# Optimization experiments

Measured on AMD Instinct MI355X. Metric: run time of the kernel, lower is better.

The kernel has to match this reference:

```python
import jax, jax.numpy as jnp
import numpy as np

EPS = 1e-5

def ter_quant(w):
    # BitNet b1.58 absmean ternary quantization: scale by mean(|W|), round to {-1,0,1}, rescale.
    gamma = jnp.mean(jnp.abs(w)) + EPS
    wq = jnp.clip(jnp.round(w / gamma), -1.0, 1.0) * gamma
    return wq

def setup_inputs() -> dict:
    key = jax.random.key(0)
    k_x, k_w1, k_w2 = jax.random.split(key, 3)
    B, S, D, H = 64, 197, 768, 3072
    x = jax.random.normal(k_x, (B, S, D), dtype=jnp.float32)
    w1 = jax.random.normal(k_w1, (H, D), dtype=jnp.float32) * (1.0 / np.sqrt(D))
    b1 = jnp.zeros((H,), dtype=jnp.float32)
    w2 = jax.random.normal(k_w2, (D, H), dtype=jnp.float32) * (1.0 / np.sqrt(H))
    b2 = jnp.zeros((D,), dtype=jnp.float32)
    return {"x": x, "w1": w1, "b1": b1, "w2": w2, "b2": b2}

def reference(x, w1, b1, w2, b2):
    # fc1: ternary-quantized linear, exact GELU, fc2: ternary-quantized linear (dropout p=0 is identity)
    h = jnp.einsum('bsd,hd->bsh', x, ter_quant(w1)) + b1
    h = jax.nn.gelu(h, approximate=False)
    y = jnp.einsum('bsh,dh->bsd', h, ter_quant(w2)) + b2
    return y
```

## Files before the change

kernel.cpp:

```cpp
#include <hip/hip_runtime.h>
#include <hip/hip_bf16.h>
#include <math.h>

typedef __bf16 bf16_t;
typedef __bf16 bf16x8 __attribute__((ext_vector_type(8)));
typedef float f32x4 __attribute__((ext_vector_type(4)));

#define QEPS 1e-5

__device__ __forceinline__ void gload_lds16(const void* g, void* l) {
  __builtin_amdgcn_global_load_lds((const __attribute__((address_space(1))) void*)g,
                                   (__attribute__((address_space(3))) void*)l, 16, 0, 0);
}

__device__ __forceinline__ float gelu_exact(float x) {
  float a = x * 0.7071067811865476f;
  float s = fabsf(a);
  float t = __builtin_amdgcn_rcpf(__builtin_fmaf(0.3275911f, s, 1.0f));
  float p = __builtin_fmaf(1.061405429f, t, -1.453152027f);
  p = __builtin_fmaf(p, t, 1.421413741f);
  p = __builtin_fmaf(p, t, -0.284496736f);
  p = __builtin_fmaf(p, t, 0.254829592f);
  p = p * t;
  float e = __expf(-s * s);
  float er = copysignf(__builtin_fmaf(-p, e, 1.0f), a);
  return 0.5f * x * (1.0f + er);
}

__global__ void reduce_part_kernel(const float* __restrict__ w1, const float* __restrict__ w2,
                                   int n, double* __restrict__ part) {
  const bool second = blockIdx.x >= 256;
  const float* __restrict__ w = second ? w2 : w1;
  const int b = second ? blockIdx.x - 256 : blockIdx.x;
  double s = 0.0;
  const int stride = 256 * 256 * 4;
  for (int i = (b * 256 + threadIdx.x) * 4; i < n; i += stride) {
    float4 v = *(const float4*)(w + i);
    s += (double)fabsf(v.x) + (double)fabsf(v.y) + (double)fabsf(v.z) + (double)fabsf(v.w);
  }
  for (int off = 32; off > 0; off >>= 1)
    s += __shfl_down(s, off, 64);
  __shared__ double ls[4];
  int lane = threadIdx.x & 63, wv = threadIdx.x >> 6;
  if (lane == 0) ls[wv] = s;
  __syncthreads();
  if (threadIdx.x == 0) part[blockIdx.x] = ls[0] + ls[1] + ls[2] + ls[3];
}

__global__ void prep_kernel(const float* __restrict__ w1, const float* __restrict__ w2,
                            const float* __restrict__ x, const double* __restrict__ part,
                            double* __restrict__ gammas, bf16_t* __restrict__ q1,
                            bf16_t* __restrict__ q2, bf16_t* __restrict__ xb) {
  const int tid = threadIdx.x;
  const int b = blockIdx.x;
  if (b < 2304) {
    const bool second = b >= 1152;
    double p = part[(second ? 256 : 0) + tid];
    for (int off = 32; off > 0; off >>= 1)
      p += __shfl_down(p, off, 64);
    __shared__ double red[4];
    if ((tid & 63) == 0) red[tid >> 6] = p;
    __syncthreads();
    const double g = (red[0] + red[1] + red[2] + red[3]) / 2359296.0 + QEPS;
    if (tid == 0 && (b == 0 || b == 1152)) gammas[second ? 1 : 0] = g;
    const double rg = 1.0 / g;
    const int gchunk = (second ? b - 1152 : b) * 256 + tid;
    const int tile = gchunk >> 10, cidx = gchunk & 1023;
    const int r = cidx >> 3, slot = cidx & 7, kc = slot ^ (r & 7);
    int row, col, C;
    const float* __restrict__ W;
    if (second) { C = 3072; W = w2; row = (tile / 48) * 128 + r; col = (tile % 48) * 64 + kc * 8; }
    else        { C = 768;  W = w1; row = (tile / 12) * 128 + r; col = (tile % 12) * 64 + kc * 8; }
    const float4 v0 = *(const float4*)(W + (size_t)row * C + col);
    const float4 v1 = *(const float4*)(W + (size_t)row * C + col + 4);
    bf16x8 o;
    o[0] = (bf16_t)(float)fmin(1.0, fmax(-1.0, rint((double)v0.x * rg)));
    o[1] = (bf16_t)(float)fmin(1.0, fmax(-1.0, rint((double)v0.y * rg)));
    o[2] = (bf16_t)(float)fmin(1.0, fmax(-1.0, rint((double)v0.z * rg)));
    o[3] = (bf16_t)(float)fmin(1.0, fmax(-1.0, rint((double)v0.w * rg)));
    o[4] = (bf16_t)(float)fmin(1.0, fmax(-1.0, rint((double)v1.x * rg)));
    o[5] = (bf16_t)(float)fmin(1.0, fmax(-1.0, rint((double)v1.y * rg)));
    o[6] = (bf16_t)(float)fmin(1.0, fmax(-1.0, rint((double)v1.z * rg)));
    o[7] = (bf16_t)(float)fmin(1.0, fmax(-1.0, rint((double)v1.w * rg)));
    *(bf16x8*)((second ? q2 : q1) + (size_t)gchunk * 8) = o;
  } else {
    const int gchunk = (b - 2304) * 256 + tid;
    const int tile = gchunk >> 10, cidx = gchunk & 1023;
    const int r = cidx >> 3, slot = cidx & 7, kc = slot ^ (r & 7);
    const int row = (tile / 12) * 128 + r;
    const int col = (tile % 12) * 64 + kc * 8;
    bf16x8 o;
    if (row < 12608) {
      const float4 v0 = *(const float4*)(x + (size_t)row * 768 + col);
      const float4 v1 = *(const float4*)(x + (size_t)row * 768 + col + 4);
      o[0] = (bf16_t)v0.x; o[1] = (bf16_t)v0.y; o[2] = (bf16_t)v0.z; o[3] = (bf16_t)v0.w;
      o[4] = (bf16_t)v1.x; o[5] = (bf16_t)v1.y; o[6] = (bf16_t)v1.z; o[7] = (bf16_t)v1.w;
    } else {
      o = bf16x8{};
    }
    *(bf16x8*)(xb + (size_t)gchunk * 8) = o;
  }
}

template <int EPI>
__global__ __launch_bounds__(256, 2)
void gemm_db(const bf16_t* __restrict__ A, const bf16_t* __restrict__ B,
             const float* __restrict__ bias, const double* __restrict__ gptr,
             void* __restrict__ Cout, int nkt, int gx, int Mvalid, int aux) {
  extern __shared__ bf16_t sm[];

  const int G = gridDim.x;
  const int f = blockIdx.x;
  const int xcd = f & 7;
  const int idx = f >> 3;
  const int q8 = G >> 3, r8 = G & 7;
  const int t = xcd * q8 + (xcd < r8 ? xcd : r8) + idx;
  const int bx = t % gx;
  const int by = t / gx;

  const int tid = threadIdx.x;
  const int lane = tid & 63;
  const int wave = tid >> 6;
  const int row16 = lane & 15;
  const int quad = lane >> 4;
  const int wr = (wave >> 1) * 64;
  const int wc = (wave & 1) * 64;
  const int sw0 = (quad ^ (row16 & 7)) * 8;
  const int sw1 = sw0 ^ 32;

  const bf16_t* const gA = A + (size_t)by * nkt * 8192;
  const bf16_t* const gB = B + (size_t)bx * nkt * 8192;

  f32x4 acc[4][4] = {};

  const int o8 = tid * 8;
  const int w512 = wave * 512;

#pragma unroll
  for (int l = 0; l < 4; l++) {
    gload_lds16(gA + l * 2048 + o8, sm + l * 2048 + w512);
    gload_lds16(gB + l * 2048 + o8, sm + 16384 + l * 2048 + w512);
  }
  __syncthreads();

  int p = 0;
  for (int T = 0; T < nkt; T++) {
    if (T + 1 < nkt) {
      const bf16_t* sa = gA + (size_t)(T + 1) * 8192;
      const bf16_t* sb = gB + (size_t)(T + 1) * 8192;
      bf16_t* dA = sm + (p ^ 1) * 8192;
      bf16_t* dB = sm + 16384 + (p ^ 1) * 8192;
#pragma unroll
      for (int l = 0; l < 4; l++) {
        gload_lds16(sa + l * 2048 + o8, dA + l * 2048 + w512);
        gload_lds16(sb + l * 2048 + o8, dB + l * 2048 + w512);
      }
    }
    const bf16_t* sA = sm + p * 8192;
    const bf16_t* sB = sm + 16384 + p * 8192;
    bf16x8 aw[4][2], bw[4][2];
#pragma unroll
    for (int i = 0; i < 4; i++) {
      const bf16_t* pr = sA + (wr + i * 16 + row16) * 64;
      aw[i][0] = *(const bf16x8*)(pr + sw0);
      aw[i][1] = *(const bf16x8*)(pr + sw1);
    }
#pragma unroll
    for (int j = 0; j < 4; j++) {
      const bf16_t* pr = sB + (wc + j * 16 + row16) * 64;
      bw[j][0] = *(const bf16x8*)(pr + sw0);
      bw[j][1] = *(const bf16x8*)(pr + sw1);
    }
#pragma unroll
    for (int i = 0; i < 4; i++)
#pragma unroll
      for (int j = 0; j < 4; j++) {
        acc[i][j] = __builtin_amdgcn_mfma_f32_16x16x32_bf16(aw[i][0], bw[j][0], acc[i][j], 0, 0, 0);
        acc[i][j] = __builtin_amdgcn_mfma_f32_16x16x32_bf16(aw[i][1], bw[j][1], acc[i][j], 0, 0, 0);
      }
    __syncthreads();
    p ^= 1;
  }

  const float gamma = (float)gptr[0];
  float bv[4];
#pragma unroll
  for (int j = 0; j < 4; j++) bv[j] = bias[bx * 128 + wc + j * 16 + row16];

  if constexpr (EPI == 0) {
    constexpr int SEW = 136;
    bf16_t* sE = sm;
#pragma unroll
    for (int i = 0; i < 4; i++) {
      const int rb = wr + i * 16 + quad * 4;
#pragma unroll
      for (int j = 0; j < 4; j++) {
        const int col = wc + j * 16 + row16;
#pragma unroll
        for (int r = 0; r < 4; r++)
          sE[(rb + r) * SEW + col] =
              (bf16_t)gelu_exact(__builtin_fmaf(gamma, acc[i][j][r], bv[j]));
      }
    }
    __syncthreads();
    bf16_t* hb = (bf16_t*)Cout;
#pragma unroll
    for (int kh = 0; kh < 2; kh++) {
      bf16_t* ht = hb + ((size_t)by * aux + bx * 2 + kh) * 8192;
#pragma unroll
      for (int n = 0; n < 4; n++) {
        const int g = n * 256 + tid;
        const int r = g >> 3, slot = g & 7, c = slot ^ (r & 7);
        *(bf16x8*)(ht + g * 8) = *(const bf16x8*)(sE + r * SEW + kh * 64 + c * 8);
      }
    }
  } else {
    float* outp = (float*)Cout;
#pragma unroll
    for (int j = 0; j < 4; j++) {
      const int col = bx * 128 + wc + j * 16 + row16;
#pragma unroll
      for (int i = 0; i < 4; i++) {
        const int rb = by * 128 + wr + i * 16 + quad * 4;
#pragma unroll
        for (int r = 0; r < 4; r++)
          if (rb + r < Mvalid)
            outp[(size_t)(rb + r) * aux + col] = __builtin_fmaf(gamma, acc[i][j][r], bv[j]);
      }
    }
  }
}

extern "C" void kernel_launch(void* const* d_in, const int* in_sizes, int n_in,
                              void* d_out, int out_size, void* d_ws, size_t ws_size,
                              hipStream_t stream) {
  const float* x  = (const float*)d_in[0];
  const float* w1 = (const float*)d_in[1];
  const float* b1 = (const float*)d_in[2];
  const float* w2 = (const float*)d_in[3];
  const float* b2 = (const float*)d_in[4];
  float* out = (float*)d_out;

  const int M = 64 * 197;
  const int Mpad = 12800;
  const int D = 768, H = 3072;
  const int nW = H * D;

  char* ws = (char*)d_ws;
  double* part = (double*)ws;
  double* gammas = (double*)(ws + 4096);
  bf16_t* xb  = (bf16_t*)(ws + 4096 + 256);
  bf16_t* w1q = xb + (size_t)Mpad * D;
  bf16_t* w2q = w1q + (size_t)H * D;
  bf16_t* hb  = w2q + (size_t)D * H;

  static bool attr_done = false;
  if (!attr_done) {
    (void)hipFuncSetAttribute(reinterpret_cast<const void*>(&gemm_db<0>),
                              hipFuncAttributeMaxDynamicSharedMemorySize, 65536);
    (void)hipFuncSetAttribute(reinterpret_cast<const void*>(&gemm_db<1>),
                              hipFuncAttributeMaxDynamicSharedMemorySize, 65536);
    attr_done = true;
  }

  reduce_part_kernel<<<512, 256, 0, stream>>>(w1, w2, nW, part);
  prep_kernel<<<2304 + 4800, 256, 0, stream>>>(w1, w2, x, part, gammas, w1q, w2q, xb);

  gemm_db<0><<<100 * 24, 256, 65536, stream>>>(xb, w1q, b1, gammas + 0, hb, 12, 24, M, H / 64);
  gemm_db<1><<<100 * 6, 256, 65536, stream>>>(hb, w2q, b2, gammas + 1, out, 48, 6, M, D);
}
```

Measured before the change: 275.0 us.

## Load A operand directly into registers, stage only B in LDS

The GEMM kernel now reads the A tile straight from global memory into registers, double-buffered across k-steps, and stages only the B tile in LDS, which halves LDS use to 32KB of static shared memory. That allows launch bounds of 4 blocks per CU instead of 2. The x conversion now writes A unswizzled in plain row-major chunks, and the GELU epilogue writes h in the same layout, in two halves to fit the smaller LDS. The trade-off is uncoalesced-ish global A loads per lane and higher register pressure under the 4-block bound.

```diff
diff --git a/kernel.cpp b/kernel.cpp
--- a/kernel.cpp
+++ b/kernel.cpp
@@ -86,9 +86,9 @@
   } else {
     const int gchunk = (b - 2304) * 256 + tid;
     const int tile = gchunk >> 10, cidx = gchunk & 1023;
-    const int r = cidx >> 3, slot = cidx & 7, kc = slot ^ (r & 7);
+    const int r = cidx >> 3, slot = cidx & 7;
     const int row = (tile / 12) * 128 + r;
-    const int col = (tile % 12) * 64 + kc * 8;
+    const int col = (tile % 12) * 64 + slot * 8;
     bf16x8 o;
     if (row < 12608) {
       const float4 v0 = *(const float4*)(x + (size_t)row * 768 + col);
@@ -103,11 +103,11 @@
 }
 
 template <int EPI>
-__global__ __launch_bounds__(256, 2)
-void gemm_db(const bf16_t* __restrict__ A, const bf16_t* __restrict__ B,
+__global__ __launch_bounds__(256, 4)
+void gemm_ar(const bf16_t* __restrict__ A, const bf16_t* __restrict__ B,
              const float* __restrict__ bias, const double* __restrict__ gptr,
              void* __restrict__ Cout, int nkt, int gx, int Mvalid, int aux) {
-  extern __shared__ bf16_t sm[];
+  __shared__ bf16_t sm[2][8192];
 
   const int G = gridDim.x;
   const int f = blockIdx.x;
@@ -125,61 +125,58 @@
   const int quad = lane >> 4;
   const int wr = (wave >> 1) * 64;
   const int wc = (wave & 1) * 64;
+
+  const bf16_t* const Ab = A + (size_t)by * nkt * 8192;
+  const bf16_t* const Bb = B + (size_t)bx * nkt * 8192;
+
+  const int abase = (wr + row16) * 64 + quad * 8;
   const int sw0 = (quad ^ (row16 & 7)) * 8;
-  const int sw1 = sw0 ^ 32;
-
-  const bf16_t* const gA = A + (size_t)by * nkt * 8192;
-  const bf16_t* const gB = B + (size_t)bx * nkt * 8192;
+  const int boffA = (wc + row16) * 64 + sw0;
+  const int boffB = (wc + row16) * 64 + (sw0 ^ 32);
 
   f32x4 acc[4][4] = {};
-
-  const int o8 = tid * 8;
-  const int w512 = wave * 512;
-
-#pragma unroll
-  for (int l = 0; l < 4; l++) {
-    gload_lds16(gA + l * 2048 + o8, sm + l * 2048 + w512);
-    gload_lds16(gB + l * 2048 + o8, sm + 16384 + l * 2048 + w512);
-  }
-  __syncthreads();
-
-  int p = 0;
-  for (int T = 0; T < nkt; T++) {
-    if (T + 1 < nkt) {
-      const bf16_t* sa = gA + (size_t)(T + 1) * 8192;
-      const bf16_t* sb = gB + (size_t)(T + 1) * 8192;
-      bf16_t* dA = sm + (p ^ 1) * 8192;
-      bf16_t* dB = sm + 16384 + (p ^ 1) * 8192;
-#pragma unroll
-      for (int l = 0; l < 4; l++) {
-        gload_lds16(sa + l * 2048 + o8, dA + l * 2048 + w512);
-        gload_lds16(sb + l * 2048 + o8, dB + l * 2048 + w512);
-      }
-    }
-    const bf16_t* sA = sm + p * 8192;
-    const bf16_t* sB = sm + 16384 + p * 8192;
-    bf16x8 aw[4][2], bw[4][2];
-#pragma unroll
-    for (int i = 0; i < 4; i++) {
-      const bf16_t* pr = sA + (wr + i * 16 + row16) * 64;
-      aw[i][0] = *(const bf16x8*)(pr + sw0);
-      aw[i][1] = *(const bf16x8*)(pr + sw1);
-    }
-#pragma unroll
-    for (int j = 0; j < 4; j++) {
-      const bf16_t* pr = sB + (wc + j * 16 + row16) * 64;
-      bw[j][0] = *(const bf16x8*)(pr + sw0);
-      bw[j][1] = *(const bf16x8*)(pr + sw1);
-    }
-#pragma unroll
-    for (int i = 0; i < 4; i++)
-#pragma unroll
-      for (int j = 0; j < 4; j++) {
-        acc[i][j] = __builtin_amdgcn_mfma_f32_16x16x32_bf16(aw[i][0], bw[j][0], acc[i][j], 0, 0, 0);
-        acc[i][j] = __builtin_amdgcn_mfma_f32_16x16x32_bf16(aw[i][1], bw[j][1], acc[i][j], 0, 0, 0);
-      }
-    __syncthreads();
-    p ^= 1;
+  bf16x8 awA[8], awB[8], bw[8];
+
+#define LOADA_(dst, tt) do { \
+    const bf16_t* ap_ = Ab + (size_t)(tt) * 8192 + abase; \
+    _Pragma("unroll") for (int i_ = 0; i_ < 4; i_++) { \
+      dst[2 * i_]     = *(const bf16x8*)(ap_ + i_ * 1024); \
+      dst[2 * i_ + 1] = *(const bf16x8*)(ap_ + i_ * 1024 + 32); } } while (0)
+#define STAGEB_(tt, bufv) do { \
+    const bf16_t* sp_ = Bb + (size_t)(tt) * 8192; \
+    bf16_t* dp_ = sm[bufv]; \
+    _Pragma("unroll") for (int l_ = 0; l_ < 4; l_++) \
+      gload_lds16(sp_ + l_ * 2048 + tid * 8, dp_ + l_ * 2048 + wave * 512); } while (0)
+#define LOADB_(bufv) do { \
+    const bf16_t* b0_ = sm[bufv] + boffA; \
+    const bf16_t* b1_ = sm[bufv] + boffB; \
+    _Pragma("unroll") for (int j_ = 0; j_ < 4; j_++) { \
+      bw[2 * j_]     = *(const bf16x8*)(b0_ + j_ * 1024); \
+      bw[2 * j_ + 1] = *(const bf16x8*)(b1_ + j_ * 1024); } } while (0)
+#define MFMAALL_(awc) do { \
+    _Pragma("unroll") for (int i_ = 0; i_ < 4; i_++) \
+    _Pragma("unroll") for (int j_ = 0; j_ < 4; j_++) { \
+      acc[i_][j_] = __builtin_amdgcn_mfma_f32_16x16x32_bf16(awc[2*i_],   bw[2*j_],   acc[i_][j_], 0, 0, 0); \
+      acc[i_][j_] = __builtin_amdgcn_mfma_f32_16x16x32_bf16(awc[2*i_+1], bw[2*j_+1], acc[i_][j_], 0, 0, 0); } } while (0)
+#define BODY_(tt, curb, awc, awn) do { \
+    if ((tt) + 1 < nkt) STAGEB_((tt) + 1, (curb) ^ 1); \
+    __builtin_amdgcn_sched_barrier(0); \
+    if ((tt) + 1 < nkt) LOADA_(awn, (tt) + 1); \
+    LOADB_(curb); \
+    MFMAALL_(awc); \
+    if ((tt) + 1 < nkt) { \
+      asm volatile("s_waitcnt vmcnt(8)" ::: "memory"); \
+      __builtin_amdgcn_s_barrier(); } } while (0)
+
+  STAGEB_(0, 0);
+  __builtin_amdgcn_sched_barrier(0);
+  LOADA_(awA, 0);
+  asm volatile("s_waitcnt vmcnt(8)" ::: "memory");
+  __builtin_amdgcn_s_barrier();
+
+  for (int T = 0; T < nkt; T += 2) {
+    BODY_(T, 0, awA, awB);
+    BODY_(T + 1, 1, awB, awA);
   }
 
   const float gamma = (float)gptr[0];
@@ -189,30 +186,36 @@
 
   if constexpr (EPI == 0) {
     constexpr int SEW = 136;
-    bf16_t* sE = sm;
-#pragma unroll
-    for (int i = 0; i < 4; i++) {
-      const int rb = wr + i * 16 + quad * 4;
-#pragma unroll
-      for (int j = 0; j < 4; j++) {
-        const int col = wc + j * 16 + row16;
-#pragma unroll
-        for (int r = 0; r < 4; r++)
-          sE[(rb + r) * SEW + col] =
-              (bf16_t)gelu_exact(__builtin_fmaf(gamma, acc[i][j][r], bv[j]));
+    bf16_t* sE = &sm[0][0];
+    bf16_t* hbp = (bf16_t*)Cout;
+    __syncthreads();
+#pragma unroll
+    for (int h = 0; h < 2; h++) {
+#pragma unroll
+      for (int u = 0; u < 2; u++) {
+        const int i = 2 * h + u;
+        const int rb = wr + i * 16 + quad * 4;
+#pragma unroll
+        for (int j = 0; j < 4; j++) {
+          const int col = wc + j * 16 + row16;
+#pragma unroll
+          for (int r = 0; r < 4; r++) {
+            const int row = rb + r;
+            const int e = (row & 31) + ((row & 64) >> 1);
+            sE[e * SEW + col] = (bf16_t)gelu_exact(__builtin_fmaf(gamma, acc[i][j][r], bv[j]));
+          }
+        }
       }
-    }
-    __syncthreads();
-    bf16_t* hb = (bf16_t*)Cout;
-#pragma unroll
-    for (int kh = 0; kh < 2; kh++) {
-      bf16_t* ht = hb + ((size_t)by * aux + bx * 2 + kh) * 8192;
+      __syncthreads();
 #pragma unroll
       for (int n = 0; n < 4; n++) {
         const int g = n * 256 + tid;
-        const int r = g >> 3, slot = g & 7, c = slot ^ (r & 7);
-        *(bf16x8*)(ht + g * 8) = *(const bf16x8*)(sE + r * SEW + kh * 64 + c * 8);
+        const int e = g >> 4, ch = g & 15;
+        const int grow = (e & 31) + ((e & 32) << 1) + 32 * h;
+        const size_t off = ((size_t)by * aux + bx * 2 + (ch >> 3)) * 8192 + (grow * 8 + (ch & 7)) * 8;
+        *(bf16x8*)(hbp + off) = *(const bf16x8*)(sE + e * SEW + ch * 8);
       }
+      __syncthreads();
     }
   } else {
     float* outp = (float*)Cout;
@@ -229,6 +232,11 @@
       }
     }
   }
+#undef LOADA_
+#undef STAGEB_
+#undef LOADB_
+#undef MFMAALL_
+#undef BODY_
 }
 
 extern "C" void kernel_launch(void* const* d_in, const int* in_sizes, int n_in,
@@ -254,18 +262,9 @@
   bf16_t* w2q = w1q + (size_t)H * D;
   bf16_t* hb  = w2q + (size_t)D * H;
 
-  static bool attr_done = false;
-  if (!attr_done) {
-    (void)hipFuncSetAttribute(reinterpret_cast<const void*>(&gemm_db<0>),
-                              hipFuncAttributeMaxDynamicSharedMemorySize, 65536);
-    (void)hipFuncSetAttribute(reinterpret_cast<const void*>(&gemm_db<1>),
-                              hipFuncAttributeMaxDynamicSharedMemorySize, 65536);
-    attr_done = true;
-  }
-
   reduce_part_kernel<<<512, 256, 0, stream>>>(w1, w2, nW, part);
   prep_kernel<<<2304 + 4800, 256, 0, stream>>>(w1, w2, x, part, gammas, w1q, w2q, xb);
 
-  gemm_db<0><<<100 * 24, 256, 65536, stream>>>(xb, w1q, b1, gammas + 0, hb, 12, 24, M, H / 64);
-  gemm_db<1><<<100 * 6, 256, 65536, stream>>>(hb, w2q, b2, gammas + 1, out, 48, 6, M, D);
-}
+  gemm_ar<0><<<100 * 24, 256, 0, stream>>>(xb, w1q, b1, gammas + 0, hb, 12, 24, M, H / 64);
+  gemm_ar<1><<<100 * 6, 256, 0, stream>>>(hb, w2q, b2, gammas + 1, out, 48, 6, M, D);
+}
```

Measured after the change: 853.4 us. 210% more time.

## Switch GEMMs to K=32 tiles with triple-buffered LDS pipeline

Applied to the files above, without the earlier changes.

The pre-tiled bf16 layouts for x, quantized weights and the hidden activation shrink from 64-wide to 32-wide K tiles with a 4-way swizzle. The GEMM kernel now uses 48KB of static LDS with three stages and explicit vmcnt waits, so loads can run two tiles ahead. Occupancy is raised to 3 blocks per CU, and M padding drops from 12800 to 12672 so fewer wasted row tiles are launched. The cost is more barriers per unit of K work and smaller MFMA batches between synchronizations.

```diff
diff --git a/kernel.cpp b/kernel.cpp
--- a/kernel.cpp
+++ b/kernel.cpp
@@ -65,14 +65,14 @@
     if (tid == 0 && (b == 0 || b == 1152)) gammas[second ? 1 : 0] = g;
     const double rg = 1.0 / g;
     const int gchunk = (second ? b - 1152 : b) * 256 + tid;
-    const int tile = gchunk >> 10, cidx = gchunk & 1023;
-    const int r = cidx >> 3, slot = cidx & 7, kc = slot ^ (r & 7);
-    int row, col, C;
-    const float* __restrict__ W;
-    if (second) { C = 3072; W = w2; row = (tile / 48) * 128 + r; col = (tile % 48) * 64 + kc * 8; }
-    else        { C = 768;  W = w1; row = (tile / 12) * 128 + r; col = (tile % 12) * 64 + kc * 8; }
-    const float4 v0 = *(const float4*)(W + (size_t)row * C + col);
-    const float4 v1 = *(const float4*)(W + (size_t)row * C + col + 4);
+    const int tile = gchunk >> 9, cidx = gchunk & 511;
+    const int r = cidx >> 2, slot = cidx & 3, cch = slot ^ (r & 3);
+    int row, colbase, C;
+    if (second) { C = 3072; row = (tile / 96) * 128 + r; colbase = (tile % 96) * 32 + cch * 8; }
+    else        { C = 768;  row = (tile / 24) * 128 + r; colbase = (tile % 24) * 32 + cch * 8; }
+    const float* __restrict__ W = second ? w2 : w1;
+    const float4 v0 = *(const float4*)(W + (size_t)row * C + colbase);
+    const float4 v1 = *(const float4*)(W + (size_t)row * C + colbase + 4);
     bf16x8 o;
     o[0] = (bf16_t)(float)fmin(1.0, fmax(-1.0, rint((double)v0.x * rg)));
     o[1] = (bf16_t)(float)fmin(1.0, fmax(-1.0, rint((double)v0.y * rg)));
@@ -85,14 +85,14 @@
     *(bf16x8*)((second ? q2 : q1) + (size_t)gchunk * 8) = o;
   } else {
     const int gchunk = (b - 2304) * 256 + tid;
-    const int tile = gchunk >> 10, cidx = gchunk & 1023;
-    const int r = cidx >> 3, slot = cidx & 7, kc = slot ^ (r & 7);
-    const int row = (tile / 12) * 128 + r;
-    const int col = (tile % 12) * 64 + kc * 8;
+    const int tile = gchunk >> 9, cidx = gchunk & 511;
+    const int r = cidx >> 2, slot = cidx & 3, cch = slot ^ (r & 3);
+    const int row = (tile / 24) * 128 + r;
+    const int colbase = (tile % 24) * 32 + cch * 8;
     bf16x8 o;
     if (row < 12608) {
-      const float4 v0 = *(const float4*)(x + (size_t)row * 768 + col);
-      const float4 v1 = *(const float4*)(x + (size_t)row * 768 + col + 4);
+      const float4 v0 = *(const float4*)(x + (size_t)row * 768 + colbase);
+      const float4 v1 = *(const float4*)(x + (size_t)row * 768 + colbase + 4);
       o[0] = (bf16_t)v0.x; o[1] = (bf16_t)v0.y; o[2] = (bf16_t)v0.z; o[3] = (bf16_t)v0.w;
       o[4] = (bf16_t)v1.x; o[5] = (bf16_t)v1.y; o[6] = (bf16_t)v1.z; o[7] = (bf16_t)v1.w;
     } else {
@@ -103,11 +103,13 @@
 }
 
 template <int EPI>
-__global__ __launch_bounds__(256, 2)
-void gemm_db(const bf16_t* __restrict__ A, const bf16_t* __restrict__ B,
+__global__ __launch_bounds__(256, 3)
+void gemm_t3(const bf16_t* __restrict__ A, const bf16_t* __restrict__ B,
              const float* __restrict__ bias, const double* __restrict__ gptr,
              void* __restrict__ Cout, int nkt, int gx, int Mvalid, int aux) {
-  extern __shared__ bf16_t sm[];
+  __shared__ bf16_t sm[24576];
+  bf16_t* const sA = sm;
+  bf16_t* const sB = sm + 12288;
 
   const int G = gridDim.x;
   const int f = blockIdx.x;
@@ -125,62 +127,55 @@
   const int quad = lane >> 4;
   const int wr = (wave >> 1) * 64;
   const int wc = (wave & 1) * 64;
-  const int sw0 = (quad ^ (row16 & 7)) * 8;
-  const int sw1 = sw0 ^ 32;
-
-  const bf16_t* const gA = A + (size_t)by * nkt * 8192;
-  const bf16_t* const gB = B + (size_t)bx * nkt * 8192;
-
-  f32x4 acc[4][4] = {};
-
+  const int sw = (quad ^ (row16 & 3)) * 8;
+
+  const bf16_t* const gA = A + (size_t)by * nkt * 4096;
+  const bf16_t* const gB = B + (size_t)bx * nkt * 4096;
   const int o8 = tid * 8;
   const int w512 = wave * 512;
 
-#pragma unroll
-  for (int l = 0; l < 4; l++) {
-    gload_lds16(gA + l * 2048 + o8, sm + l * 2048 + w512);
-    gload_lds16(gB + l * 2048 + o8, sm + 16384 + l * 2048 + w512);
-  }
-  __syncthreads();
-
-  int p = 0;
-  for (int T = 0; T < nkt; T++) {
-    if (T + 1 < nkt) {
-      const bf16_t* sa = gA + (size_t)(T + 1) * 8192;
-      const bf16_t* sb = gB + (size_t)(T + 1) * 8192;
-      bf16_t* dA = sm + (p ^ 1) * 8192;
-      bf16_t* dB = sm + 16384 + (p ^ 1) * 8192;
-#pragma unroll
-      for (int l = 0; l < 4; l++) {
-        gload_lds16(sa + l * 2048 + o8, dA + l * 2048 + w512);
-        gload_lds16(sb + l * 2048 + o8, dB + l * 2048 + w512);
-      }
-    }
-    const bf16_t* sA = sm + p * 8192;
-    const bf16_t* sB = sm + 16384 + p * 8192;
-    bf16x8 aw[4][2], bw[4][2];
-#pragma unroll
-    for (int i = 0; i < 4; i++) {
-      const bf16_t* pr = sA + (wr + i * 16 + row16) * 64;
-      aw[i][0] = *(const bf16x8*)(pr + sw0);
-      aw[i][1] = *(const bf16x8*)(pr + sw1);
-    }
-#pragma unroll
-    for (int j = 0; j < 4; j++) {
-      const bf16_t* pr = sB + (wc + j * 16 + row16) * 64;
-      bw[j][0] = *(const bf16x8*)(pr + sw0);
-      bw[j][1] = *(const bf16x8*)(pr + sw1);
-    }
-#pragma unroll
-    for (int i = 0; i < 4; i++)
-#pragma unroll
-      for (int j = 0; j < 4; j++) {
-        acc[i][j] = __builtin_amdgcn_mfma_f32_16x16x32_bf16(aw[i][0], bw[j][0], acc[i][j], 0, 0, 0);
-        acc[i][j] = __builtin_amdgcn_mfma_f32_16x16x32_bf16(aw[i][1], bw[j][1], acc[i][j], 0, 0, 0);
-      }
-    __syncthreads();
-    p ^= 1;
-  }
+  f32x4 acc[4][4] = {};
+
+#define STG_(T, buf) do { \
+    const bf16_t* sa_ = gA + (size_t)(T) * 4096; \
+    const bf16_t* sb_ = gB + (size_t)(T) * 4096; \
+    gload_lds16(sa_ + o8,        sA + (buf) * 4096 + w512); \
+    gload_lds16(sa_ + 2048 + o8, sA + (buf) * 4096 + 2048 + w512); \
+    gload_lds16(sb_ + o8,        sB + (buf) * 4096 + w512); \
+    gload_lds16(sb_ + 2048 + o8, sB + (buf) * 4096 + 2048 + w512); } while (0)
+#define CMP_(buf) do { \
+    const bf16_t* a_ = sA + (buf) * 4096; \
+    const bf16_t* b_ = sB + (buf) * 4096; \
+    bf16x8 afr[4], bfr[4]; \
+    _Pragma("unroll") for (int i_ = 0; i_ < 4; i_++) \
+      afr[i_] = *(const bf16x8*)&a_[(wr + i_ * 16 + row16) * 32 + sw]; \
+    _Pragma("unroll") for (int j_ = 0; j_ < 4; j_++) \
+      bfr[j_] = *(const bf16x8*)&b_[(wc + j_ * 16 + row16) * 32 + sw]; \
+    _Pragma("unroll") for (int i_ = 0; i_ < 4; i_++) \
+    _Pragma("unroll") for (int j_ = 0; j_ < 4; j_++) \
+      acc[i_][j_] = __builtin_amdgcn_mfma_f32_16x16x32_bf16(afr[i_], bfr[j_], acc[i_][j_], 0, 0, 0); \
+    } while (0)
+#define WB4_ do { asm volatile("s_waitcnt vmcnt(4)" ::: "memory"); \
+                  __builtin_amdgcn_sched_barrier(0); \
+                  __builtin_amdgcn_s_barrier(); \
+                  __builtin_amdgcn_sched_barrier(0); } while (0)
+#define WB0_ do { asm volatile("s_waitcnt vmcnt(0)" ::: "memory"); \
+                  __builtin_amdgcn_sched_barrier(0); \
+                  __builtin_amdgcn_s_barrier(); \
+                  __builtin_amdgcn_sched_barrier(0); } while (0)
+
+  STG_(0, 0);
+  STG_(1, 1);
+  WB4_;
+
+  for (int T = 0; T < nkt - 3; T += 3) {
+    STG_(T + 2, 2); CMP_(0); WB4_;
+    STG_(T + 3, 0); CMP_(1); WB4_;
+    STG_(T + 4, 1); CMP_(2); WB4_;
+  }
+  STG_(nkt - 1, 2); CMP_(0); WB4_;
+  CMP_(1); WB0_;
+  CMP_(2);
 
   const float gamma = (float)gptr[0];
   float bv[4];
@@ -190,6 +185,8 @@
   if constexpr (EPI == 0) {
     constexpr int SEW = 136;
     bf16_t* sE = sm;
+    bf16_t* hbp = (bf16_t*)Cout;
+    __syncthreads();
 #pragma unroll
     for (int i = 0; i < 4; i++) {
       const int rb = wr + i * 16 + quad * 4;
@@ -203,16 +200,14 @@
       }
     }
     __syncthreads();
-    bf16_t* hb = (bf16_t*)Cout;
-#pragma unroll
-    for (int kh = 0; kh < 2; kh++) {
-      bf16_t* ht = hb + ((size_t)by * aux + bx * 2 + kh) * 8192;
-#pragma unroll
-      for (int n = 0; n < 4; n++) {
-        const int g = n * 256 + tid;
-        const int r = g >> 3, slot = g & 7, c = slot ^ (r & 7);
-        *(bf16x8*)(ht + g * 8) = *(const bf16x8*)(sE + r * SEW + kh * 64 + c * 8);
-      }
+#pragma unroll
+    for (int n = 0; n < 8; n++) {
+      const int gc = n * 256 + tid;
+      const int r = gc >> 4, c = gc & 15;
+      const int kt_o = bx * 4 + (c >> 2);
+      const int slot = (c & 3) ^ (r & 3);
+      *(bf16x8*)&hbp[((size_t)(by * aux + kt_o)) * 4096 + r * 32 + slot * 8] =
+          *(const bf16x8*)&sE[r * SEW + c * 8];
     }
   } else {
     float* outp = (float*)Cout;
@@ -229,6 +224,10 @@
       }
     }
   }
+#undef STG_
+#undef CMP_
+#undef WB4_
+#undef WB0_
 }
 
 extern "C" void kernel_launch(void* const* d_in, const int* in_sizes, int n_in,
@@ -242,7 +241,7 @@
   float* out = (float*)d_out;
 
   const int M = 64 * 197;
-  const int Mpad = 12800;
+  const int Mpad = 12672;
   const int D = 768, H = 3072;
   const int nW = H * D;
 
@@ -254,18 +253,9 @@
   bf16_t* w2q = w1q + (size_t)H * D;
   bf16_t* hb  = w2q + (size_t)D * H;
 
-  static bool attr_done = false;
-  if (!attr_done) {
-    (void)hipFuncSetAttribute(reinterpret_cast<const void*>(&gemm_db<0>),
-                              hipFuncAttributeMaxDynamicSharedMemorySize, 65536);
-    (void)hipFuncSetAttribute(reinterpret_cast<const void*>(&gemm_db<1>),
-                              hipFuncAttributeMaxDynamicSharedMemorySize, 65536);
-    attr_done = true;
-  }
-
   reduce_part_kernel<<<512, 256, 0, stream>>>(w1, w2, nW, part);
-  prep_kernel<<<2304 + 4800, 256, 0, stream>>>(w1, w2, x, part, gammas, w1q, w2q, xb);
-
-  gemm_db<0><<<100 * 24, 256, 65536, stream>>>(xb, w1q, b1, gammas + 0, hb, 12, 24, M, H / 64);
-  gemm_db<1><<<100 * 6, 256, 65536, stream>>>(hb, w2q, b2, gammas + 1, out, 48, 6, M, D);
-}
+  prep_kernel<<<2304 + 4752, 256, 0, stream>>>(w1, w2, x, part, gammas, w1q, w2q, xb);
+
+  gemm_t3<0><<<99 * 24, 256, 0, stream>>>(xb, w1q, b1, gammas + 0, hb, 24, 24, M, H / 32);
+  gemm_t3<1><<<99 * 6, 256, 0, stream>>>(hb, w2q, b2, gammas + 1, out, 96, 6, M, D);
+}
```

Measured after the change: 253.1 us. 1.09x faster.
